# Kernel tuning notes

Measured on AMD Instinct MI355X. Metric: run time of the kernel, lower is better.

The kernel has to match this reference:

```python
import jax, jax.numpy as jnp
import numpy as np

N_NODES = 50000
E_TRAIN = 800000
E_POS = 200000
E_NEG = 200000
F_IN = 128


def gcn_conv(x, W, b, src, dst, n):
    """PyG-style GCNConv: add self-loops, symmetric deg^{-1/2} norm, linear, scatter-add."""
    loop = jnp.arange(n, dtype=src.dtype)
    s = jnp.concatenate([src, loop])  # [E+N]
    d = jnp.concatenate([dst, loop])
    deg = jax.ops.segment_sum(jnp.ones(d.shape, dtype=x.dtype), d, num_segments=n)
    dis = jax.lax.rsqrt(jnp.maximum(deg, 1.0))  # deg >= 1 due to self-loops
    norm = dis[s] * dis[d]  # [E+N]
    h = x @ W  # [N, out]
    msg = h[s] * norm[:, None]  # gather + per-edge scale
    return jax.ops.segment_sum(msg, d, num_segments=n) + b


def reference(x, train_pos_edge_index, pos_edge_index, neg_edge_index, W1, b1, W2, b2, W3, b3):
    src, dst = train_pos_edge_index[0], train_pos_edge_index[1]
    h = jax.nn.relu(gcn_conv(x, W1, b1, src, dst, N_NODES))
    h = jax.nn.relu(gcn_conv(h, W2, b2, src, dst, N_NODES))
    h = gcn_conv(h, W3, b3, src, dst, N_NODES)
    te = jnp.concatenate([pos_edge_index, neg_edge_index], axis=-1)  # [2, E_pos+E_neg]
    x_j = h[te[0]]
    x_i = h[te[1]]
    return jnp.einsum('ef,ef->e', x_i, x_j)


def setup_inputs() -> dict:
    key = jax.random.key(0)
    ks = jax.random.split(key, 10)
    glorot = lambda k, fi, fo: jax.random.normal(k, (fi, fo), dtype=jnp.float32) * np.float32(np.sqrt(2.0 / (fi + fo)))
    return {
        'x': jax.random.normal(ks[0], (N_NODES, F_IN), dtype=jnp.float32),
        'train_pos_edge_index': jax.random.randint(ks[1], (2, E_TRAIN), 0, N_NODES, dtype=jnp.int32),
        'pos_edge_index': jax.random.randint(ks[2], (2, E_POS), 0, N_NODES, dtype=jnp.int32),
        'neg_edge_index': jax.random.randint(ks[3], (2, E_NEG), 0, N_NODES, dtype=jnp.int32),
        'W1': glorot(ks[4], F_IN, 256), 'b1': jnp.zeros((256,), jnp.float32),
        'W2': glorot(ks[5], 256, 128), 'b2': jnp.zeros((128,), jnp.float32),
        'W3': glorot(ks[6], 128, 64), 'b3': jnp.zeros((64,), jnp.float32),
    }
```

## Files before the change

### kernel.cpp

```cpp
#include <hip/hip_runtime.h>
#include <math.h>

#define N_NODES 50000
#define E_TRAIN 800000
#define E_POS 200000
#define E_NEG 200000

#define NBUCK 196
#define BSTRIDE 5120
#define PSTRIDE 6912
#define PARTA_BLOCKS 196


__device__ inline void split_bf16(float f, short& h, short& l) {
    unsigned u = __float_as_uint(f);
    h = (short)(u >> 16);
    float rem = f - __uint_as_float(u & 0xFFFF0000u);
    l = (short)(__float_as_uint(rem) >> 16);
}

__device__ inline unsigned short f2bf_rne(float f) {
    unsigned u = __float_as_uint(f);
    unsigned r = u + 0x7FFFu + ((u >> 16) & 1u);
    return (unsigned short)(r >> 16);
}

__device__ inline float bf2f(unsigned short h) {
    return __uint_as_float(((unsigned)h) << 16);
}

#define WTOT (128 * 256 + 256 * 128 + 128 * 64)


__global__ void partA_prep_kernel(
        const int* __restrict__ src, const int* __restrict__ dst,
        int* __restrict__ gcount, unsigned int* __restrict__ temp, int e,
        const float* __restrict__ W1, short* __restrict__ W1h, short* __restrict__ W1l,
        const float* __restrict__ W2, short* __restrict__ W2h, short* __restrict__ W2l,
        const float* __restrict__ W3, short* __restrict__ W3h, short* __restrict__ W3l,
        const float* __restrict__ x, unsigned short* __restrict__ xb, int n4) {
    __shared__ int hist[NBUCK];
    __shared__ int base[NBUCK];
    __shared__ int lcur[NBUCK];
    int tid = threadIdx.x;
    if (blockIdx.x < PARTA_BLOCKS) {
        for (int i = tid; i < NBUCK; i += 256) hist[i] = 0;
        __syncthreads();
        int start = blockIdx.x * 4096;
        int stop = min(start + 4096, e);
        for (int i = start + tid; i < stop; i += 256)
            atomicAdd(&hist[dst[i] >> 8], 1);
        __syncthreads();
        for (int i = tid; i < NBUCK; i += 256) {
            base[i] = atomicAdd(&gcount[i], hist[i]);
            lcur[i] = 0;
        }
        __syncthreads();
        for (int i = start + tid; i < stop; i += 256) {
            int d = dst[i];
            int b = d >> 8;
            int off = atomicAdd(&lcur[b], 1);
            temp[(size_t)b * BSTRIDE + base[b] + off] = ((unsigned)src[i] << 8) | (unsigned)(d & 255);
        }
    } else {
        int i = (blockIdx.x - PARTA_BLOCKS) * 256 + tid;
        if (i < WTOT) {
            const float* W; short *Wh, *Wl; int K, N;
            if (i < 128 * 256) { W = W1; Wh = W1h; Wl = W1l; K = 128; N = 256; }
            else if (i < 128 * 256 + 256 * 128) { i -= 128 * 256; W = W2; Wh = W2h; Wl = W2l; K = 256; N = 128; }
            else { i -= 128 * 256 + 256 * 128; W = W3; Wh = W3h; Wl = W3l; K = 128; N = 64; }
            int k = i / N, n = i - k * N;
            short h, l;
            split_bf16(W[i], h, l);
            Wh[(size_t)n * K + k] = h;
            Wl[(size_t)n * K + k] = l;
        } else {
            int j = i - WTOT;
            if (j < n4) {
                float4 v = ((const float4*)x)[j];
                ushort4 o;
                o.x = f2bf_rne(v.x); o.y = f2bf_rne(v.y);
                o.z = f2bf_rne(v.z); o.w = f2bf_rne(v.w);
                ((ushort4*)xb)[j] = o;
            }
        }
    }
}


__global__ void partB_kernel(const unsigned int* __restrict__ temp,
                             const int* __restrict__ gcount,
                             float* __restrict__ dis, int* __restrict__ offs, int* __restrict__ ends,
                             unsigned short* __restrict__ csr) {
    __shared__ int cnt[256];
    __shared__ int loc[256];
    __shared__ int cursor[256];
    int b = blockIdx.x;
    int t = threadIdx.x;
    int total = gcount[b];
    size_t tbase = (size_t)b * BSTRIDE;
    cnt[t] = 0;
    __syncthreads();
    for (int i = t; i < total; i += 256)
        atomicAdd(&cnt[temp[tbase + i] & 255], 1);
    __syncthreads();
    int c = cnt[t];
    int pc = (c + 7) & ~7;
    loc[t] = pc;
    __syncthreads();
    for (int d = 1; d < 256; d <<= 1) {
        int u = 0;
        if (t >= d) u = loc[t - d];
        __syncthreads();
        if (t >= d) loc[t] += u;
        __syncthreads();
    }
    int excl = loc[t] - pc;
    int node = b * 256 + t;
    int gstart = b * PSTRIDE + excl;
    if (node < N_NODES) {
        dis[node] = 1.0f / sqrtf((float)(c + 1));
        offs[node] = gstart;
        ends[node] = gstart + pc;
    }
    cursor[t] = gstart;
    __syncthreads();
    for (int i = t; i < total; i += 256) {
        unsigned v = temp[tbase + i];
        int pos = atomicAdd(&cursor[v & 255], 1);
        csr[pos] = (unsigned short)(v >> 8);
    }
    __syncthreads();
    for (int j = c; j < pc; j++)
        csr[gstart + j] = 0xFFFFu;
}

__global__ void wdis_kernel(unsigned short* __restrict__ csr,
                            const float* __restrict__ dis,
                            float* __restrict__ wdis, int n) {
    int i = blockIdx.x * blockDim.x + threadIdx.x;
    if (i < n) {
        unsigned short s = csr[i];
        if (s == 0xFFFFu) { csr[i] = 0; wdis[i] = 0.f; }
        else wdis[i] = dis[s];
    }
}


typedef short bf16x8 __attribute__((ext_vector_type(8)));
typedef float f32x4 __attribute__((ext_vector_type(4)));

template<int BN, bool BR, bool OBF>
__global__ __launch_bounds__(512) void gemm_fulln_kernel(
        const short* __restrict__ Ah, const short* __restrict__ Al,
        const short* __restrict__ Bth, const short* __restrict__ Btl,
        const float* __restrict__ bias,
        short* __restrict__ Ch, short* __restrict__ Cl,
        unsigned short* __restrict__ Cb,
        int M, int K) {
    constexpr int NI = BN / 16;
    constexpr int BCH = BN * 4;
    constexpr int BP = (BCH + 511) / 512;
    constexpr size_t BSZ = (size_t)2 * BN * 40 * 2;
    constexpr size_t TSZ = (size_t)8 * 16 * 68 * 4;
    __shared__ __align__(16) char smem[BSZ > TSZ ? BSZ : TSZ];
    short* Bhi = (short*)smem;
    short* Blo = (short*)(smem + (size_t)BN * 40 * 2);
    float* tr  = (float*)smem;

    int tid = threadIdx.x;
    int lane = tid & 63;
    int wv = tid >> 6;
    int brow = blockIdx.x * 128;
    int m_lane = lane & 15;
    int kgrp = lane >> 4;

    int myrow = brow + wv * 16 + m_lane;
    if (myrow >= M) myrow = M - 1;
    const short* Aph = &Ah[(size_t)myrow * K + kgrp * 8];
    const short* Apl = &Al[(size_t)myrow * K + kgrp * 8];

    f32x4 acc[NI];
    #pragma unroll
    for (int i = 0; i < NI; i++) acc[i] = (f32x4){0.f, 0.f, 0.f, 0.f};

    int4 bhReg[BP], blReg[BP];
    bf16x8 ahN, alN, ahC, alC;

    auto loadB = [&](int k0) {
        #pragma unroll
        for (int p = 0; p < BP; p++) {
            int idx = p * 512 + tid;
            if (idx < BCH) {
                int col = idx >> 2;
                int kc = idx & 3;
                size_t o = (size_t)col * K + k0 + kc * 8;
                bhReg[p] = *(const int4*)&Bth[o];
                blReg[p] = *(const int4*)&Btl[o];
            }
        }
    };
    auto loadA = [&](int k0) {
        ahN = *(const bf16x8*)&Aph[k0];
        alN = *(const bf16x8*)&Apl[k0];
    };

    loadB(0); loadA(0);

    for (int k0 = 0; k0 < K; k0 += 32) {
        ahC = ahN; alC = alN;
        #pragma unroll
        for (int p = 0; p < BP; p++) {
            int idx = p * 512 + tid;
            if (idx < BCH) {
                int col = idx >> 2;
                int kc = idx & 3;
                *(int4*)&Bhi[col * 40 + kc * 8] = bhReg[p];
                *(int4*)&Blo[col * 40 + kc * 8] = blReg[p];
            }
        }
        __syncthreads();

        if (k0 + 32 < K) { loadB(k0 + 32); loadA(k0 + 32); }

        #pragma unroll
        for (int ni = 0; ni < NI; ni++) {
            int boff = (ni * 16 + m_lane) * 40 + kgrp * 8;
            bf16x8 bh = *(const bf16x8*)&Bhi[boff];
            bf16x8 bl = *(const bf16x8*)&Blo[boff];
            acc[ni] = __builtin_amdgcn_mfma_f32_16x16x32_bf16(ahC, bh, acc[ni], 0, 0, 0);
            acc[ni] = __builtin_amdgcn_mfma_f32_16x16x32_bf16(alC, bh, acc[ni], 0, 0, 0);
            acc[ni] = __builtin_amdgcn_mfma_f32_16x16x32_bf16(ahC, bl, acc[ni], 0, 0, 0);
        }
        __syncthreads();
    }

    #pragma unroll
    for (int c = 0; c < NI / 4; c++) {
        #pragma unroll
        for (int q = 0; q < 4; q++) {
            int ni = c * 4 + q;
            float bb = 0.f;
            if (BR) bb = bias[ni * 16 + m_lane];
            #pragma unroll
            for (int reg = 0; reg < 4; reg++) {
                float v = acc[ni][reg];
                if (BR) v = fmaxf(v + bb, 0.f);
                tr[wv * 1088 + (kgrp * 4 + reg) * 68 + q * 16 + m_lane] = v;
            }
        }
        #pragma unroll
        for (int j = 0; j < 4; j++) {
            int r = (lane >> 4) + j * 4;
            int g = lane & 15;
            float4 v = *(const float4*)&tr[wv * 1088 + r * 68 + g * 4];
            int row = brow + wv * 16 + r;
            if (row < M) {
                if (OBF) {
                    ushort4 o;
                    o.x = f2bf_rne(v.x); o.y = f2bf_rne(v.y);
                    o.z = f2bf_rne(v.z); o.w = f2bf_rne(v.w);
                    *(ushort4*)&Cb[(size_t)row * BN + c * 64 + g * 4] = o;
                } else {
                    short4 oh, ol;
                    short h, l;
                    split_bf16(v.x, h, l); oh.x = h; ol.x = l;
                    split_bf16(v.y, h, l); oh.y = h; ol.y = l;
                    split_bf16(v.z, h, l); oh.z = h; ol.z = l;
                    split_bf16(v.w, h, l); oh.w = h; ol.w = l;
                    *(short4*)&Ch[(size_t)row * BN + c * 64 + g * 4] = oh;
                    *(short4*)&Cl[(size_t)row * BN + c * 64 + g * 4] = ol;
                }
            }
        }
    }
}


#define AGG_WAVES 12800
#define AGG_BLOCKS (AGG_WAVES / 4)

template<int F, bool RELU, bool BIAS, int OUTM>
__global__ void aggregate_bf16_kernel(const unsigned short* __restrict__ xb,
                                      short* __restrict__ outh,
                                      short* __restrict__ outl,
                                      float* __restrict__ outf,
                                      const float* __restrict__ dis,
                                      const int* __restrict__ starts,
                                      const int* __restrict__ ends,
                                      const unsigned short* __restrict__ csr_src,
                                      const float* __restrict__ wdis,
                                      const float* __restrict__ bias,
                                      int n) {
    int wid = (blockIdx.x * blockDim.x + threadIdx.x) >> 6;
    int lane = threadIdx.x & 63;
    constexpr int VPT = F / 64;

    for (int v = wid; v < n; v += AGG_WAVES) {
        float dv = dis[v];
        float acc[VPT];
        if constexpr (VPT == 2) {
            ushort2 sv = *(const ushort2*)&xb[(size_t)v * F + lane * 2];
            acc[0] = bf2f(sv.x) * dv;
            acc[1] = bf2f(sv.y) * dv;
        } else {
            acc[0] = bf2f(xb[(size_t)v * F + lane]) * dv;
        }
        int s = __builtin_amdgcn_readfirstlane(starts[v]);
        int e = __builtin_amdgcn_readfirstlane(ends[v]);
        for (int p = s; p < e; p += 8) {
            int4 c0 = *(const int4*)&csr_src[p];
            float4 w0 = *(const float4*)&wdis[p];
            float4 w1 = *(const float4*)&wdis[p + 4];
            int u[8];
            u[0] = (unsigned)c0.x & 0xFFFF; u[1] = (unsigned)c0.x >> 16;
            u[2] = (unsigned)c0.y & 0xFFFF; u[3] = (unsigned)c0.y >> 16;
            u[4] = (unsigned)c0.z & 0xFFFF; u[5] = (unsigned)c0.z >> 16;
            u[6] = (unsigned)c0.w & 0xFFFF; u[7] = (unsigned)c0.w >> 16;
            float w[8];
            w[0] = w0.x; w[1] = w0.y; w[2] = w0.z; w[3] = w0.w;
            w[4] = w1.x; w[5] = w1.y; w[6] = w1.z; w[7] = w1.w;
            if constexpr (VPT == 2) {
                ushort2 g[8];
                #pragma unroll
                for (int q = 0; q < 8; q++)
                    g[q] = *(const ushort2*)&xb[(size_t)u[q] * F + lane * 2];
                #pragma unroll
                for (int q = 0; q < 8; q++) {
                    acc[0] += bf2f(g[q].x) * w[q];
                    acc[1] += bf2f(g[q].y) * w[q];
                }
            } else {
                unsigned short g[8];
                #pragma unroll
                for (int q = 0; q < 8; q++)
                    g[q] = xb[(size_t)u[q] * F + lane];
                #pragma unroll
                for (int q = 0; q < 8; q++) acc[0] += bf2f(g[q]) * w[q];
            }
        }
        size_t base = (size_t)v * F + lane * VPT;
        if constexpr (OUTM == 1) {
            #pragma unroll
            for (int i = 0; i < VPT; i++) {
                float r = acc[i] * dv;
                if (BIAS) r += bias[lane * VPT + i];
                if (RELU) r = fmaxf(r, 0.f);
                outf[base + i] = r;
            }
        } else {
            if constexpr (VPT == 2) {
                float r0 = acc[0] * dv, r1 = acc[1] * dv;
                if (BIAS) { r0 += bias[lane * 2]; r1 += bias[lane * 2 + 1]; }
                if (RELU) { r0 = fmaxf(r0, 0.f); r1 = fmaxf(r1, 0.f); }
                short h0, l0, h1, l1;
                split_bf16(r0, h0, l0);
                split_bf16(r1, h1, l1);
                short2 oh; oh.x = h0; oh.y = h1;
                short2 ol; ol.x = l0; ol.y = l1;
                *(short2*)&outh[base] = oh;
                *(short2*)&outl[base] = ol;
            } else {
                float r = acc[0] * dv;
                if (BIAS) r += bias[lane];
                if (RELU) r = fmaxf(r, 0.f);
                short h, l;
                split_bf16(r, h, l);
                outh[base] = h;
                outl[base] = l;
            }
        }
    }
}


__global__ void dot_kernel(const float* __restrict__ h,
                           const int* __restrict__ pos, const int* __restrict__ neg,
                           float* __restrict__ out) {
    int gw = (blockIdx.x * blockDim.x + threadIdx.x) >> 6;
    int lane = threadIdx.x & 63;
    int sub = lane >> 4;
    int pl = lane & 15;
    int e = gw * 4 + sub;
    if (e >= E_POS + E_NEG) return;
    int i0, i1;
    if (e < E_POS) { i0 = pos[e]; i1 = pos[E_POS + e]; }
    else { int t = e - E_POS; i0 = neg[t]; i1 = neg[E_NEG + t]; }
    float4 a = *(const float4*)&h[(size_t)i0 * 64 + pl * 4];
    float4 b = *(const float4*)&h[(size_t)i1 * 64 + pl * 4];
    float v = a.x * b.x + a.y * b.y + a.z * b.z + a.w * b.w;
    v += __shfl_xor(v, 1, 64);
    v += __shfl_xor(v, 2, 64);
    v += __shfl_xor(v, 4, 64);
    v += __shfl_xor(v, 8, 64);
    if (pl == 0) out[e] = v;
}


extern "C" void kernel_launch(void* const* d_in, const int* in_sizes, int n_in,
                              void* d_out, int out_size, void* d_ws, size_t ws_size,
                              hipStream_t stream) {
    const float* x  = (const float*)d_in[0];
    const int* tei  = (const int*)d_in[1];
    const int* pos  = (const int*)d_in[2];
    const int* neg  = (const int*)d_in[3];
    const float* W1 = (const float*)d_in[4];
    const float* b1 = (const float*)d_in[5];
    const float* W2 = (const float*)d_in[6];
    const float* b2 = (const float*)d_in[7];
    const float* W3 = (const float*)d_in[8];
    const float* b3 = (const float*)d_in[9];
    float* out = (float*)d_out;

    const int* src = tei;
    const int* dst = tei + E_TRAIN;

    char* ws = (char*)d_ws;
    size_t off = 0;
    auto alloc = [&](size_t bytes) -> void* {
        void* p = ws + off;
        off = (off + bytes + 255) & ~(size_t)255;
        return p;
    };
    unsigned short* xb = (unsigned short*)alloc((size_t)N_NODES * 128 * 2);
    short* aggXh       = (short*)alloc((size_t)N_NODES * 128 * 2);
    short* aggXl       = (short*)alloc((size_t)N_NODES * 128 * 2);
    short* h1h         = (short*)alloc((size_t)N_NODES * 256 * 2);
    short* h1l         = (short*)alloc((size_t)N_NODES * 256 * 2);
    unsigned short* xw2b = (unsigned short*)alloc((size_t)N_NODES * 128 * 2);
    short* h2h         = (short*)alloc((size_t)N_NODES * 128 * 2);
    short* h2l         = (short*)alloc((size_t)N_NODES * 128 * 2);
    unsigned short* xw3b = (unsigned short*)alloc((size_t)N_NODES * 64 * 2);
    float* h3          = (float*)alloc((size_t)N_NODES * 64 * 4);
    float* dis  = (float*)alloc(N_NODES * 4);
    int* offs   = (int*)alloc(N_NODES * 4);
    int* ends   = (int*)alloc(N_NODES * 4);
    int* gcount = (int*)alloc(NBUCK * 4);
    unsigned int* temp  = (unsigned int*)alloc((size_t)NBUCK * BSTRIDE * 4);
    unsigned short* csr = (unsigned short*)alloc((size_t)NBUCK * PSTRIDE * 2);
    float* wdis         = (float*)alloc((size_t)NBUCK * PSTRIDE * 4);
    short* Wt1h = (short*)alloc((size_t)128 * 256 * 2);
    short* Wt1l = (short*)alloc((size_t)128 * 256 * 2);
    short* Wt2h = (short*)alloc((size_t)256 * 128 * 2);
    short* Wt2l = (short*)alloc((size_t)256 * 128 * 2);
    short* Wt3h = (short*)alloc((size_t)128 * 64 * 2);
    short* Wt3l = (short*)alloc((size_t)128 * 64 * 2);
    (void)ws_size; (void)n_in; (void)in_sizes; (void)out_size;

    const int n4 = N_NODES * 128 / 4;

    hipMemsetAsync(gcount, 0, NBUCK * 4, stream);
    {
        int prep_blocks = (WTOT + n4 + 255) / 256;
        partA_prep_kernel<<<PARTA_BLOCKS + prep_blocks, 256, 0, stream>>>(
            src, dst, gcount, temp, E_TRAIN,
            W1, Wt1h, Wt1l, W2, Wt2h, Wt2l, W3, Wt3h, Wt3l, x, xb, n4);
    }
    partB_kernel<<<NBUCK, 256, 0, stream>>>(temp, gcount, dis, offs, ends, csr);
    {
        int ncsr = NBUCK * PSTRIDE;
        wdis_kernel<<<(ncsr + 255) / 256, 256, 0, stream>>>(csr, dis, wdis, ncsr);
    }

    const int GB = (N_NODES + 127) / 128;

    aggregate_bf16_kernel<128, false, false, 0><<<AGG_BLOCKS, 256, 0, stream>>>(
        xb, aggXh, aggXl, nullptr, dis, offs, ends, csr, wdis, nullptr, N_NODES);
    gemm_fulln_kernel<256, true, false><<<GB, 512, 0, stream>>>(
        aggXh, aggXl, Wt1h, Wt1l, b1, h1h, h1l, nullptr, N_NODES, 128);

    gemm_fulln_kernel<128, false, true><<<GB, 512, 0, stream>>>(
        h1h, h1l, Wt2h, Wt2l, nullptr, nullptr, nullptr, xw2b, N_NODES, 256);
    aggregate_bf16_kernel<128, true, true, 0><<<AGG_BLOCKS, 256, 0, stream>>>(
        xw2b, h2h, h2l, nullptr, dis, offs, ends, csr, wdis, b2, N_NODES);

    gemm_fulln_kernel<64, false, true><<<GB, 512, 0, stream>>>(
        h2h, h2l, Wt3h, Wt3l, nullptr, nullptr, nullptr, xw3b, N_NODES, 128);
    aggregate_bf16_kernel<64, false, true, 1><<<AGG_BLOCKS, 256, 0, stream>>>(
        xw3b, nullptr, nullptr, h3, dis, offs, ends, csr, wdis, b3, N_NODES);

    const int DOT_WAVES = (E_POS + E_NEG + 3) / 4;
    dot_kernel<<<(DOT_WAVES + 3) / 4, 256, 0, stream>>>(h3, pos, neg, out);
}
```

Measured before the change: 297.1 us.

## Fuse layer-1 and layer-2 GEMMs into one kernel, keeping hidden activations on-chip

Replaces the two back-to-back GEMM launches (aggX·W1+b1 with relu, then h1·W2) with a single kernel. Each wave keeps its 16x256 layer-1 result in registers, applies bias and relu, splits it into bf16 hi/lo through an LDS transpose and feeds it straight into the second MFMA chain. This removes the write and re-read of the 50000x256 split-bf16 h1 buffers and one launch. In exchange, the layer-2 weights are read directly from global memory per wave rather than staged in LDS, and register pressure rises with both accumulator sets live.

```diff
diff --git a/kernel.cpp b/kernel.cpp
--- a/kernel.cpp
+++ b/kernel.cpp
@@ -146,9 +146,162 @@
     }
 }
 
-
 typedef short bf16x8 __attribute__((ext_vector_type(8)));
 typedef float f32x4 __attribute__((ext_vector_type(4)));
+
+
+__global__ __launch_bounds__(512) void gemm12_kernel(
+        const short* __restrict__ Ah, const short* __restrict__ Al,
+        const short* __restrict__ B1h, const short* __restrict__ B1l,
+        const float* __restrict__ bias1,
+        const short* __restrict__ B2h, const short* __restrict__ B2l,
+        unsigned short* __restrict__ Cb,
+        int M) {
+    constexpr int K1 = 128;
+    constexpr int BN1 = 256;
+    constexpr int NI1 = 16;
+    constexpr int K2 = 256;
+    constexpr int NI2 = 8;
+    constexpr int BCH = BN1 * 4;
+    constexpr int BP = BCH / 512;
+    __shared__ __align__(16) char smem[40960];
+    short* Bhi = (short*)smem;
+    short* Blo = (short*)(smem + (size_t)BN1 * 40 * 2);
+    float* tr  = (float*)smem;
+
+    int tid = threadIdx.x;
+    int lane = tid & 63;
+    int wv = tid >> 6;
+    int brow = blockIdx.x * 128;
+    int m_lane = lane & 15;
+    int kgrp = lane >> 4;
+
+    int myrow = brow + wv * 16 + m_lane;
+    if (myrow >= M) myrow = M - 1;
+    const short* Aph = &Ah[(size_t)myrow * K1 + kgrp * 8];
+    const short* Apl = &Al[(size_t)myrow * K1 + kgrp * 8];
+
+    f32x4 acc[NI1];
+    #pragma unroll
+    for (int i = 0; i < NI1; i++) acc[i] = (f32x4){0.f, 0.f, 0.f, 0.f};
+
+    int4 bhReg[BP], blReg[BP];
+    bf16x8 ahN, alN, ahC, alC;
+
+    auto loadB = [&](int k0) {
+        #pragma unroll
+        for (int p = 0; p < BP; p++) {
+            int idx = p * 512 + tid;
+            int col = idx >> 2;
+            int kc = idx & 3;
+            size_t o = (size_t)col * K1 + k0 + kc * 8;
+            bhReg[p] = *(const int4*)&B1h[o];
+            blReg[p] = *(const int4*)&B1l[o];
+        }
+    };
+    auto loadA = [&](int k0) {
+        ahN = *(const bf16x8*)&Aph[k0];
+        alN = *(const bf16x8*)&Apl[k0];
+    };
+
+    loadB(0); loadA(0);
+
+    for (int k0 = 0; k0 < K1; k0 += 32) {
+        ahC = ahN; alC = alN;
+        #pragma unroll
+        for (int p = 0; p < BP; p++) {
+            int idx = p * 512 + tid;
+            int col = idx >> 2;
+            int kc = idx & 3;
+            *(int4*)&Bhi[col * 40 + kc * 8] = bhReg[p];
+            *(int4*)&Blo[col * 40 + kc * 8] = blReg[p];
+        }
+        __syncthreads();
+
+        if (k0 + 32 < K1) { loadB(k0 + 32); loadA(k0 + 32); }
+
+        #pragma unroll
+        for (int ni = 0; ni < NI1; ni++) {
+            int boff = (ni * 16 + m_lane) * 40 + kgrp * 8;
+            bf16x8 bh = *(const bf16x8*)&Bhi[boff];
+            bf16x8 bl = *(const bf16x8*)&Blo[boff];
+            acc[ni] = __builtin_amdgcn_mfma_f32_16x16x32_bf16(ahC, bh, acc[ni], 0, 0, 0);
+            acc[ni] = __builtin_amdgcn_mfma_f32_16x16x32_bf16(alC, bh, acc[ni], 0, 0, 0);
+            acc[ni] = __builtin_amdgcn_mfma_f32_16x16x32_bf16(ahC, bl, acc[ni], 0, 0, 0);
+        }
+        __syncthreads();
+    }
+
+    f32x4 acc2[NI2];
+    #pragma unroll
+    for (int i = 0; i < NI2; i++) acc2[i] = (f32x4){0.f, 0.f, 0.f, 0.f};
+
+    #pragma unroll
+    for (int c = 0; c < 4; c++) {
+        #pragma unroll
+        for (int q = 0; q < 4; q++) {
+            int ni = c * 4 + q;
+            float bb = bias1[ni * 16 + m_lane];
+            #pragma unroll
+            for (int reg = 0; reg < 4; reg++) {
+                float v = fmaxf(acc[ni][reg] + bb, 0.f);
+                tr[wv * 1088 + (kgrp * 4 + reg) * 68 + q * 16 + m_lane] = v;
+            }
+        }
+        #pragma unroll
+        for (int ks = 0; ks < 2; ks++) {
+            float4 f0 = *(const float4*)&tr[wv * 1088 + m_lane * 68 + ks * 32 + kgrp * 8];
+            float4 f1 = *(const float4*)&tr[wv * 1088 + m_lane * 68 + ks * 32 + kgrp * 8 + 4];
+            bf16x8 ah2, al2;
+            {
+                short h, l;
+                split_bf16(f0.x, h, l); ah2[0] = h; al2[0] = l;
+                split_bf16(f0.y, h, l); ah2[1] = h; al2[1] = l;
+                split_bf16(f0.z, h, l); ah2[2] = h; al2[2] = l;
+                split_bf16(f0.w, h, l); ah2[3] = h; al2[3] = l;
+                split_bf16(f1.x, h, l); ah2[4] = h; al2[4] = l;
+                split_bf16(f1.y, h, l); ah2[5] = h; al2[5] = l;
+                split_bf16(f1.z, h, l); ah2[6] = h; al2[6] = l;
+                split_bf16(f1.w, h, l); ah2[7] = h; al2[7] = l;
+            }
+            int kg = c * 64 + ks * 32 + kgrp * 8;
+            #pragma unroll
+            for (int ni2 = 0; ni2 < NI2; ni2++) {
+                size_t bo = (size_t)(ni2 * 16 + m_lane) * K2 + kg;
+                bf16x8 bh2 = *(const bf16x8*)&B2h[bo];
+                bf16x8 bl2 = *(const bf16x8*)&B2l[bo];
+                acc2[ni2] = __builtin_amdgcn_mfma_f32_16x16x32_bf16(ah2, bh2, acc2[ni2], 0, 0, 0);
+                acc2[ni2] = __builtin_amdgcn_mfma_f32_16x16x32_bf16(al2, bh2, acc2[ni2], 0, 0, 0);
+                acc2[ni2] = __builtin_amdgcn_mfma_f32_16x16x32_bf16(ah2, bl2, acc2[ni2], 0, 0, 0);
+            }
+        }
+    }
+
+    #pragma unroll
+    for (int c2 = 0; c2 < 2; c2++) {
+        #pragma unroll
+        for (int q = 0; q < 4; q++) {
+            int ni2 = c2 * 4 + q;
+            #pragma unroll
+            for (int reg = 0; reg < 4; reg++)
+                tr[wv * 1088 + (kgrp * 4 + reg) * 68 + q * 16 + m_lane] = acc2[ni2][reg];
+        }
+        #pragma unroll
+        for (int j = 0; j < 4; j++) {
+            int r = (lane >> 4) + j * 4;
+            int g = lane & 15;
+            float4 v = *(const float4*)&tr[wv * 1088 + r * 68 + g * 4];
+            int row = brow + wv * 16 + r;
+            if (row < M) {
+                ushort4 o;
+                o.x = f2bf_rne(v.x); o.y = f2bf_rne(v.y);
+                o.z = f2bf_rne(v.z); o.w = f2bf_rne(v.w);
+                *(ushort4*)&Cb[(size_t)row * 128 + c2 * 64 + g * 4] = o;
+            }
+        }
+    }
+}
+
 
 template<int BN, bool BR, bool OBF>
 __global__ __launch_bounds__(512) void gemm_fulln_kernel(
@@ -425,8 +578,6 @@
     unsigned short* xb = (unsigned short*)alloc((size_t)N_NODES * 128 * 2);
     short* aggXh       = (short*)alloc((size_t)N_NODES * 128 * 2);
     short* aggXl       = (short*)alloc((size_t)N_NODES * 128 * 2);
-    short* h1h         = (short*)alloc((size_t)N_NODES * 256 * 2);
-    short* h1l         = (short*)alloc((size_t)N_NODES * 256 * 2);
     unsigned short* xw2b = (unsigned short*)alloc((size_t)N_NODES * 128 * 2);
     short* h2h         = (short*)alloc((size_t)N_NODES * 128 * 2);
     short* h2l         = (short*)alloc((size_t)N_NODES * 128 * 2);
@@ -466,11 +617,9 @@
 
     aggregate_bf16_kernel<128, false, false, 0><<<AGG_BLOCKS, 256, 0, stream>>>(
         xb, aggXh, aggXl, nullptr, dis, offs, ends, csr, wdis, nullptr, N_NODES);
-    gemm_fulln_kernel<256, true, false><<<GB, 512, 0, stream>>>(
-        aggXh, aggXl, Wt1h, Wt1l, b1, h1h, h1l, nullptr, N_NODES, 128);
-
-    gemm_fulln_kernel<128, false, true><<<GB, 512, 0, stream>>>(
-        h1h, h1l, Wt2h, Wt2l, nullptr, nullptr, nullptr, xw2b, N_NODES, 256);
+    gemm12_kernel<<<GB, 512, 0, stream>>>(
+        aggXh, aggXl, Wt1h, Wt1l, b1, Wt2h, Wt2l, xw2b, N_NODES);
+
     aggregate_bf16_kernel<128, true, true, 0><<<AGG_BLOCKS, 256, 0, stream>>>(
         xw2b, h2h, h2l, nullptr, dis, offs, ends, csr, wdis, b2, N_NODES);
 
```

Result: slower. 319.4 us (+7.5%).
